# Performance work log

Measured on AMD Instinct MI355X. Metric: run time of the kernel, lower is better.

The kernel has to match this reference:

```python
import jax, jax.numpy as jnp
import numpy as np

B, S, M, D, H, L, FF = 2, 1024, 1024, 512, 8, 4, 2048
HD = D // H  # head dim 64
EPS = 1e-6   # fast_transformers linear-attention eps
LN_EPS = 1e-5


def setup_inputs() -> dict:
    key = jax.random.key(0)
    keys = iter(jax.random.split(key, 64))
    def w(shape, s=0.02):
        return jax.random.normal(next(keys), shape, dtype=jnp.float32) * s
    inp = {
        "memory": jax.random.normal(next(keys), (B, M, D), dtype=jnp.float32),
        "target": jax.random.normal(next(keys), (B, S, D), dtype=jnp.float32),
    }
    for p in ("sa", "ca"):
        for n in ("q", "k", "v", "o"):
            inp[f"{p}_W{n}"] = w((L, D, D))
            inp[f"{p}_b{n}"] = jnp.zeros((L, D), jnp.float32)
    inp["ff_W1"] = w((L, D, FF)); inp["ff_b1"] = jnp.zeros((L, FF), jnp.float32)
    inp["ff_W2"] = w((L, FF, D)); inp["ff_b2"] = jnp.zeros((L, D), jnp.float32)
    for n in ("ln1", "ln2", "ln3"):
        inp[f"{n}_g"] = jnp.ones((L, D), jnp.float32)
        inp[f"{n}_b"] = jnp.zeros((L, D), jnp.float32)
    inp["lnf_g"] = jnp.ones((D,), jnp.float32)
    inp["lnf_b"] = jnp.zeros((D,), jnp.float32)
    return inp


def _ln(x, g, b):
    m = x.mean(-1, keepdims=True)
    v = ((x - m) ** 2).mean(-1, keepdims=True)
    return (x - m) / jnp.sqrt(v + LN_EPS) * g + b


def _phi(x):  # elu feature map: elu(x) + 1
    return jax.nn.elu(x) + 1.0


def _heads(x, W, b):  # [b,s,D] -> [b,s,H,HD]
    y = x @ W + b
    return y.reshape(y.shape[0], y.shape[1], H, HD)


def _causal_linear_attn(q, k, v):
    # q,k already feature-mapped. cumulative KV state per step.
    kv = jnp.cumsum(jnp.einsum('bshd,bshm->bshdm', k, v), axis=1)  # [B,S,H,HD,HD]
    z = jnp.cumsum(k, axis=1)                                      # [B,S,H,HD]
    num = jnp.einsum('bshd,bshdm->bshm', q, kv)
    den = jnp.einsum('bshd,bshd->bsh', q, z) + EPS
    return num / den[..., None]


def _cross_linear_attn(q, k, v):
    kv = jnp.einsum('bmhd,bmhv->bhdv', k, v)  # [B,H,HD,HD]
    z = k.sum(axis=1)                          # [B,H,HD]
    num = jnp.einsum('bshd,bhdv->bshv', q, kv)
    den = jnp.einsum('bshd,bhd->bsh', q, z) + EPS
    return num / den[..., None]


def reference(memory, target,
              sa_Wq, sa_bq, sa_Wk, sa_bk, sa_Wv, sa_bv, sa_Wo, sa_bo,
              ca_Wq, ca_bq, ca_Wk, ca_bk, ca_Wv, ca_bv, ca_Wo, ca_bo,
              ff_W1, ff_b1, ff_W2, ff_b2,
              ln1_g, ln1_b, ln2_g, ln2_b, ln3_g, ln3_b, lnf_g, lnf_b):
    x = target
    for i in range(L):
        # causal linear self-attention
        q = _phi(_heads(x, sa_Wq[i], sa_bq[i]))
        k = _phi(_heads(x, sa_Wk[i], sa_bk[i]))
        v = _heads(x, sa_Wv[i], sa_bv[i])
        a = _causal_linear_attn(q, k, v).reshape(B, S, D) @ sa_Wo[i] + sa_bo[i]
        x = _ln(x + a, ln1_g[i], ln1_b[i])
        # linear cross-attention over memory
        q = _phi(_heads(x, ca_Wq[i], ca_bq[i]))
        k = _phi(_heads(memory, ca_Wk[i], ca_bk[i]))
        v = _heads(memory, ca_Wv[i], ca_bv[i])
        a = _cross_linear_attn(q, k, v).reshape(B, S, D) @ ca_Wo[i] + ca_bo[i]
        x = _ln(x + a, ln2_g[i], ln2_b[i])
        # gelu FFN
        y = jax.nn.gelu(x @ ff_W1[i] + ff_b1[i], approximate=False) @ ff_W2[i] + ff_b2[i]
        x = _ln(x + y, ln3_g[i], ln3_b[i])
    return _ln(x, lnf_g, lnf_b)
```

## Files before the change

### kernel.cpp

```cpp
#include <hip/hip_runtime.h>
#include <hip/hip_bf16.h>
#include <math.h>


typedef unsigned short u16;
typedef __bf16 bf16x8 __attribute__((ext_vector_type(8)));
typedef float f32x4v __attribute__((ext_vector_type(4)));

#define DEVI __device__ __forceinline__

DEVI float bf2f(u16 u) { return __uint_as_float(((unsigned)u) << 16); }
DEVI u16 f2bf(float f) {
  unsigned u = __float_as_uint(f);
  u += 0x7FFFu + ((u >> 16) & 1u);
  return (u16)(u >> 16);
}

__global__ __launch_bounds__(256) void transpose_f2b(
    const float* __restrict__ in, u16* __restrict__ out, int K, int N)
{
  __shared__ float tile[64 * 65];
  const size_t mat = (size_t)blockIdx.z * K * N;
  const int n0 = blockIdx.x * 64, k0 = blockIdx.y * 64;
  const int t = threadIdx.x;
#pragma unroll
  for (int p = 0; p < 16; ++p) {
    const int e = t + p * 256;
    const int lk = e >> 6, ln = e & 63;
    tile[lk * 65 + ln] = in[mat + (size_t)(k0 + lk) * N + n0 + ln];
  }
  __syncthreads();
#pragma unroll
  for (int p = 0; p < 16; ++p) {
    const int e = t + p * 256;
    const int ln = e >> 6, lk = e & 63;
    out[mat + (size_t)(n0 + ln) * K + k0 + lk] = f2bf(tile[lk * 65 + ln]);
  }
}

__global__ __launch_bounds__(256) void cast_dual(
    const float* __restrict__ in, float* __restrict__ fout, u16* __restrict__ bout)
{
  const int i = blockIdx.x * 256 + threadIdx.x;
  const float4 a = ((const float4*)in)[i * 2];
  const float4 b = ((const float4*)in)[i * 2 + 1];
  if (fout) {
    ((float4*)fout)[i * 2] = a;
    ((float4*)fout)[i * 2 + 1] = b;
  }
  ((ushort4*)bout)[i * 2]     = make_ushort4(f2bf(a.x), f2bf(a.y), f2bf(a.z), f2bf(a.w));
  ((ushort4*)bout)[i * 2 + 1] = make_ushort4(f2bf(b.x), f2bf(b.y), f2bf(b.z), f2bf(b.w));
}

template<int CDT>
__global__ __launch_bounds__(256, 4) void gemm64(
    const u16* __restrict__ A0, const u16* __restrict__ A1, const u16* __restrict__ A2,
    const u16* __restrict__ W0, const u16* __restrict__ W1, const u16* __restrict__ W2,
    const float* __restrict__ b0, const float* __restrict__ b1, const float* __restrict__ b2,
    void* __restrict__ C0, void* __restrict__ C1, void* __restrict__ C2,
    int acts, int N, int K, int lognyb)
{
  constexpr int LDT = 72;
  __shared__ __align__(16) u16 As[2][64 * LDT];
  __shared__ __align__(16) u16 Bs[2][64 * LDT];
  const int tid = threadIdx.x;
  const int by = blockIdx.y;
  const int seg = by >> lognyb;
  const int ny = by & ((1 << lognyb) - 1);
  const u16* A = seg == 0 ? A0 : (seg == 1 ? A1 : A2);
  const u16* W = seg == 0 ? W0 : (seg == 1 ? W1 : W2);
  const float* bias = seg == 0 ? b0 : (seg == 1 ? b1 : b2);
  void* Cv = seg == 0 ? C0 : (seg == 1 ? C1 : C2);
  const int act = (acts >> (2 * seg)) & 3;

  const int bm0 = blockIdx.x * 64, bn0 = ny * 64;
  const int lane = tid & 63, wid = tid >> 6;
  const int wr = wid >> 1, wc = wid & 1;
  const int l15 = lane & 15, lg = lane >> 4;
  const int srow = tid >> 2, scg = (tid & 3) * 16;
  const u16* Ap = A + (size_t)(bm0 + srow) * K + scg;
  const u16* Wp = W + (size_t)(bn0 + srow) * K + scg;

  uint4 ra0 = *(const uint4*)(Ap);
  uint4 ra1 = *(const uint4*)(Ap + 8);
  uint4 rb0 = *(const uint4*)(Wp);
  uint4 rb1 = *(const uint4*)(Wp + 8);
  *(uint4*)&As[0][srow * LDT + scg]     = ra0;
  *(uint4*)&As[0][srow * LDT + scg + 8] = ra1;
  *(uint4*)&Bs[0][srow * LDT + scg]     = rb0;
  *(uint4*)&Bs[0][srow * LDT + scg + 8] = rb1;
  __syncthreads();

  f32x4v acc[2][2] = {};
  int cur = 0;
  for (int k0 = 0; k0 < K; k0 += 64) {
    const bool more = (k0 + 64 < K);
    if (more) {
      ra0 = *(const uint4*)(Ap + k0 + 64);
      ra1 = *(const uint4*)(Ap + k0 + 72);
      rb0 = *(const uint4*)(Wp + k0 + 64);
      rb1 = *(const uint4*)(Wp + k0 + 72);
    }
    bf16x8 af[2][2], bw[2][2];
#pragma unroll
    for (int kk = 0; kk < 2; ++kk) {
#pragma unroll
      for (int mm = 0; mm < 2; ++mm)
        af[kk][mm] = *(const bf16x8*)&As[cur][(wr * 32 + mm * 16 + l15) * LDT + kk * 32 + lg * 8];
#pragma unroll
      for (int nn = 0; nn < 2; ++nn)
        bw[kk][nn] = *(const bf16x8*)&Bs[cur][(wc * 32 + nn * 16 + l15) * LDT + kk * 32 + lg * 8];
    }
#pragma unroll
    for (int kk = 0; kk < 2; ++kk)
#pragma unroll
      for (int mm = 0; mm < 2; ++mm)
#pragma unroll
        for (int nn = 0; nn < 2; ++nn)
          acc[mm][nn] = __builtin_amdgcn_mfma_f32_16x16x32_bf16(af[kk][mm], bw[kk][nn], acc[mm][nn], 0, 0, 0);
    if (more) {
      *(uint4*)&As[cur ^ 1][srow * LDT + scg]     = ra0;
      *(uint4*)&As[cur ^ 1][srow * LDT + scg + 8] = ra1;
      *(uint4*)&Bs[cur ^ 1][srow * LDT + scg]     = rb0;
      *(uint4*)&Bs[cur ^ 1][srow * LDT + scg + 8] = rb1;
    }
    __syncthreads();
    cur ^= 1;
  }
#pragma unroll
  for (int nn = 0; nn < 2; ++nn) {
    const int col = bn0 + wc * 32 + nn * 16 + l15;
    const float bv = bias[col];
#pragma unroll
    for (int mm = 0; mm < 2; ++mm) {
#pragma unroll
      for (int r = 0; r < 4; ++r) {
        const int row = bm0 + wr * 32 + mm * 16 + lg * 4 + r;
        float v = acc[mm][nn][r] + bv;
        if (act == 1) v = v > 0.f ? v + 1.f : __expf(v);
        else if (act == 2) v = 0.5f * v * (1.f + erff(v * 0.70710678f));
        if (CDT == 0) ((float*)Cv)[(size_t)row * N + col] = v;
        else          ((u16*)Cv)[(size_t)row * N + col] = f2bf(v);
      }
    }
  }
}

__global__ __launch_bounds__(256) void lin_chunk_mfma(
    const u16* __restrict__ kbuf, const u16* __restrict__ vbuf,
    float* __restrict__ KVc, float* __restrict__ zc)
{
  constexpr int LDT = 72;
  __shared__ __align__(16) u16 Kt[64 * LDT];
  __shared__ __align__(16) u16 Vt[64 * LDT];
  const int c = blockIdx.x, bh = blockIdx.y;
  const int b = bh >> 3, h = bh & 7;
  const int t = threadIdx.x;
  const size_t rowbase = (size_t)(b * 1024 + c * 64);
  const int sp = t >> 4, colq = (t & 15) * 4;
#pragma unroll
  for (int pp = 0; pp < 2; ++pp) {
    const int s0 = pp * 32 + 2 * sp;
    const ushort4 ka = *(const ushort4*)&kbuf[(rowbase + s0) * 512 + h * 64 + colq];
    const ushort4 kb_ = *(const ushort4*)&kbuf[(rowbase + s0 + 1) * 512 + h * 64 + colq];
    const ushort4 va = *(const ushort4*)&vbuf[(rowbase + s0) * 512 + h * 64 + colq];
    const ushort4 vb_ = *(const ushort4*)&vbuf[(rowbase + s0 + 1) * 512 + h * 64 + colq];
    *(unsigned*)&Kt[(colq + 0) * LDT + s0] = (unsigned)ka.x | ((unsigned)kb_.x << 16);
    *(unsigned*)&Kt[(colq + 1) * LDT + s0] = (unsigned)ka.y | ((unsigned)kb_.y << 16);
    *(unsigned*)&Kt[(colq + 2) * LDT + s0] = (unsigned)ka.z | ((unsigned)kb_.z << 16);
    *(unsigned*)&Kt[(colq + 3) * LDT + s0] = (unsigned)ka.w | ((unsigned)kb_.w << 16);
    *(unsigned*)&Vt[(colq + 0) * LDT + s0] = (unsigned)va.x | ((unsigned)vb_.x << 16);
    *(unsigned*)&Vt[(colq + 1) * LDT + s0] = (unsigned)va.y | ((unsigned)vb_.y << 16);
    *(unsigned*)&Vt[(colq + 2) * LDT + s0] = (unsigned)va.z | ((unsigned)vb_.z << 16);
    *(unsigned*)&Vt[(colq + 3) * LDT + s0] = (unsigned)va.w | ((unsigned)vb_.w << 16);
  }
  __syncthreads();
  {
    const int zd = t >> 2, zg = t & 3;
    float zp = 0.f;
#pragma unroll
    for (int ss = 0; ss < 16; ++ss) zp += bf2f(Kt[zd * LDT + zg * 16 + ss]);
    zp += __shfl_xor(zp, 1, 64);
    zp += __shfl_xor(zp, 2, 64);
    if (zg == 0) zc[(size_t)(bh * 16 + c) * 64 + zd] = zp;
  }
  const int lane = t & 63, wid = t >> 6;
  const int wr = wid >> 1, wc = wid & 1;
  const int l15 = lane & 15, lg = lane >> 4;
  bf16x8 av[2][2], bk[2][2];
#pragma unroll
  for (int kk = 0; kk < 2; ++kk) {
#pragma unroll
    for (int mm = 0; mm < 2; ++mm)
      av[kk][mm] = *(const bf16x8*)&Vt[(wr * 32 + mm * 16 + l15) * LDT + kk * 32 + lg * 8];
#pragma unroll
    for (int nn = 0; nn < 2; ++nn)
      bk[kk][nn] = *(const bf16x8*)&Kt[(wc * 32 + nn * 16 + l15) * LDT + kk * 32 + lg * 8];
  }
  f32x4v acc[2][2] = {};
#pragma unroll
  for (int kk = 0; kk < 2; ++kk)
#pragma unroll
    for (int mm = 0; mm < 2; ++mm)
#pragma unroll
      for (int nn = 0; nn < 2; ++nn)
        acc[mm][nn] = __builtin_amdgcn_mfma_f32_16x16x32_bf16(av[kk][mm], bk[kk][nn], acc[mm][nn], 0, 0, 0);
  float* kvout = KVc + (size_t)(bh * 16 + c) * 4096;
#pragma unroll
  for (int mm = 0; mm < 2; ++mm)
#pragma unroll
    for (int r = 0; r < 4; ++r) {
      const int row = wr * 32 + mm * 16 + lg * 4 + r;
#pragma unroll
      for (int nn = 0; nn < 2; ++nn) {
        const int col = wc * 32 + nn * 16 + l15;
        kvout[row * 64 + col] = acc[mm][nn][r];
      }
    }
}

__global__ __launch_bounds__(256) void lin_scan_exclusive(
    float* __restrict__ KVc, float* __restrict__ zc,
    float* __restrict__ KVtot, float* __restrict__ ztot)
{
  const int grp = blockIdx.x, bh = blockIdx.y, t = threadIdx.x;
  const size_t base = (size_t)bh * 16 * 4096 + grp * 256 + t;
  float run = 0.f;
#pragma unroll
  for (int c = 0; c < 16; ++c) {
    const float tmp = KVc[base + (size_t)c * 4096];
    KVc[base + (size_t)c * 4096] = run;
    run += tmp;
  }
  KVtot[(size_t)bh * 4096 + grp * 256 + t] = run;
  if (grp == 0 && t < 64) {
    const size_t zb = (size_t)bh * 16 * 64 + t;
    float rz = 0.f;
#pragma unroll
    for (int c = 0; c < 16; ++c) {
      const float tmp = zc[zb + c * 64];
      zc[zb + c * 64] = rz;
      rz += tmp;
    }
    ztot[bh * 64 + t] = rz;
  }
}

__global__ __launch_bounds__(256) void sa_apply_mfma(
    const u16* __restrict__ qbuf, const u16* __restrict__ kbuf,
    const u16* __restrict__ vbuf, const float* __restrict__ KVc,
    const float* __restrict__ zc, u16* __restrict__ out)
{
  constexpr int LDT = 72;
  __shared__ __align__(16) u16 Qs[64 * LDT];
  __shared__ __align__(16) u16 Ks[64 * LDT];
  __shared__ __align__(16) u16 Vt[64 * LDT];
  __shared__ __align__(16) u16 Ps[64 * LDT];
  __shared__ __align__(16) u16 KVs[64 * LDT];
  __shared__ float zp[64];
  __shared__ float den1[2][64];
  __shared__ float den2[64];
  const int c = blockIdx.x, bh = blockIdx.y;
  const int b = bh >> 3, h = bh & 7;
  const int t = threadIdx.x;
  const size_t rowbase = (size_t)(b * 1024 + c * 64);
  {
    const int srow = t >> 2, scg = (t & 3) * 16;
    *(uint4*)&Qs[srow * LDT + scg]     = *(const uint4*)&qbuf[(rowbase + srow) * 512 + h * 64 + scg];
    *(uint4*)&Qs[srow * LDT + scg + 8] = *(const uint4*)&qbuf[(rowbase + srow) * 512 + h * 64 + scg + 8];
    *(uint4*)&Ks[srow * LDT + scg]     = *(const uint4*)&kbuf[(rowbase + srow) * 512 + h * 64 + scg];
    *(uint4*)&Ks[srow * LDT + scg + 8] = *(const uint4*)&kbuf[(rowbase + srow) * 512 + h * 64 + scg + 8];
    const float* kvp = KVc + (size_t)(bh * 16 + c) * 4096 + srow * 64 + scg;
#pragma unroll
    for (int i = 0; i < 4; ++i) {
      const float4 cc = *(const float4*)&kvp[i * 4];
      *(ushort4*)&KVs[srow * LDT + scg + i * 4] = make_ushort4(f2bf(cc.x), f2bf(cc.y), f2bf(cc.z), f2bf(cc.w));
    }
  }
  {
    const int sp = t >> 4, colq = (t & 15) * 4;
#pragma unroll
    for (int pp = 0; pp < 2; ++pp) {
      const int s0 = pp * 32 + 2 * sp;
      const ushort4 va = *(const ushort4*)&vbuf[(rowbase + s0) * 512 + h * 64 + colq];
      const ushort4 vb_ = *(const ushort4*)&vbuf[(rowbase + s0 + 1) * 512 + h * 64 + colq];
      *(unsigned*)&Vt[(colq + 0) * LDT + s0] = (unsigned)va.x | ((unsigned)vb_.x << 16);
      *(unsigned*)&Vt[(colq + 1) * LDT + s0] = (unsigned)va.y | ((unsigned)vb_.y << 16);
      *(unsigned*)&Vt[(colq + 2) * LDT + s0] = (unsigned)va.z | ((unsigned)vb_.z << 16);
      *(unsigned*)&Vt[(colq + 3) * LDT + s0] = (unsigned)va.w | ((unsigned)vb_.w << 16);
    }
  }
  if (t < 64) zp[t] = zc[(size_t)(bh * 16 + c) * 64 + t];
  __syncthreads();
  {
    const int di = t >> 2, dg = t & 3;
    float p2 = 0.f;
#pragma unroll
    for (int dd = 0; dd < 16; ++dd)
      p2 += bf2f(Qs[di * LDT + dg * 16 + dd]) * zp[dg * 16 + dd];
    p2 += __shfl_xor(p2, 1, 64);
    p2 += __shfl_xor(p2, 2, 64);
    if (dg == 0) den2[di] = p2;
  }
  const int lane = t & 63, wid = t >> 6;
  const int wr = wid >> 1, wc = wid & 1;
  const int l15 = lane & 15, lg = lane >> 4;
  bf16x8 af_q[2][2], bx[2][2];
#pragma unroll
  for (int kk = 0; kk < 2; ++kk) {
#pragma unroll
    for (int mm = 0; mm < 2; ++mm)
      af_q[kk][mm] = *(const bf16x8*)&Qs[(wr * 32 + mm * 16 + l15) * LDT + kk * 32 + lg * 8];
#pragma unroll
    for (int nn = 0; nn < 2; ++nn)
      bx[kk][nn] = *(const bf16x8*)&Ks[(wc * 32 + nn * 16 + l15) * LDT + kk * 32 + lg * 8];
  }
  f32x4v s_acc[2][2] = {};
#pragma unroll
  for (int kk = 0; kk < 2; ++kk)
#pragma unroll
    for (int mm = 0; mm < 2; ++mm)
#pragma unroll
      for (int nn = 0; nn < 2; ++nn)
        s_acc[mm][nn] = __builtin_amdgcn_mfma_f32_16x16x32_bf16(af_q[kk][mm], bx[kk][nn], s_acc[mm][nn], 0, 0, 0);
#pragma unroll
  for (int mm = 0; mm < 2; ++mm)
#pragma unroll
    for (int r = 0; r < 4; ++r) {
      const int row = wr * 32 + mm * 16 + lg * 4 + r;
      float dsum = 0.f;
#pragma unroll
      for (int nn = 0; nn < 2; ++nn) {
        const int col = wc * 32 + nn * 16 + l15;
        const float val = (col <= row) ? s_acc[mm][nn][r] : 0.f;
        Ps[row * LDT + col] = f2bf(val);
        dsum += val;
      }
      dsum += __shfl_xor(dsum, 1, 64);
      dsum += __shfl_xor(dsum, 2, 64);
      dsum += __shfl_xor(dsum, 4, 64);
      dsum += __shfl_xor(dsum, 8, 64);
      if (l15 == 0) den1[wc][row] = dsum;
    }
  __syncthreads();
  bf16x8 ap[2][2];
#pragma unroll
  for (int kk = 0; kk < 2; ++kk) {
#pragma unroll
    for (int mm = 0; mm < 2; ++mm)
      ap[kk][mm] = *(const bf16x8*)&Ps[(wr * 32 + mm * 16 + l15) * LDT + kk * 32 + lg * 8];
#pragma unroll
    for (int nn = 0; nn < 2; ++nn)
      bx[kk][nn] = *(const bf16x8*)&Vt[(wc * 32 + nn * 16 + l15) * LDT + kk * 32 + lg * 8];
  }
  f32x4v o_acc[2][2] = {};
#pragma unroll
  for (int kk = 0; kk < 2; ++kk)
#pragma unroll
    for (int mm = 0; mm < 2; ++mm)
#pragma unroll
      for (int nn = 0; nn < 2; ++nn)
        o_acc[mm][nn] = __builtin_amdgcn_mfma_f32_16x16x32_bf16(ap[kk][mm], bx[kk][nn], o_acc[mm][nn], 0, 0, 0);
#pragma unroll
  for (int kk = 0; kk < 2; ++kk)
#pragma unroll
    for (int nn = 0; nn < 2; ++nn)
      bx[kk][nn] = *(const bf16x8*)&KVs[(wc * 32 + nn * 16 + l15) * LDT + kk * 32 + lg * 8];
#pragma unroll
  for (int kk = 0; kk < 2; ++kk)
#pragma unroll
    for (int mm = 0; mm < 2; ++mm)
#pragma unroll
      for (int nn = 0; nn < 2; ++nn)
        o_acc[mm][nn] = __builtin_amdgcn_mfma_f32_16x16x32_bf16(af_q[kk][mm], bx[kk][nn], o_acc[mm][nn], 0, 0, 0);
#pragma unroll
  for (int mm = 0; mm < 2; ++mm)
#pragma unroll
    for (int r = 0; r < 4; ++r) {
      const int row = wr * 32 + mm * 16 + lg * 4 + r;
      const float rden = 1.f / (den1[0][row] + den1[1][row] + den2[row] + 1e-6f);
#pragma unroll
      for (int nn = 0; nn < 2; ++nn) {
        const int col = wc * 32 + nn * 16 + l15;
        out[(rowbase + row) * 512 + h * 64 + col] = f2bf(o_acc[mm][nn][r] * rden);
      }
    }
}

__global__ __launch_bounds__(256) void ca_apply_mfma(
    const u16* __restrict__ qbuf, const float* __restrict__ KVtot,
    const float* __restrict__ ztot, u16* __restrict__ out)
{
  constexpr int LDT = 72;
  __shared__ __align__(16) u16 Qs[64 * LDT];
  __shared__ __align__(16) u16 KVs[64 * LDT];
  __shared__ float zt[64];
  __shared__ float den2[64];
  const int c = blockIdx.x, bh = blockIdx.y;
  const int b = bh >> 3, h = bh & 7;
  const int t = threadIdx.x;
  const size_t rowbase = (size_t)(b * 1024 + c * 64);
  {
    const int srow = t >> 2, scg = (t & 3) * 16;
    *(uint4*)&Qs[srow * LDT + scg]     = *(const uint4*)&qbuf[(rowbase + srow) * 512 + h * 64 + scg];
    *(uint4*)&Qs[srow * LDT + scg + 8] = *(const uint4*)&qbuf[(rowbase + srow) * 512 + h * 64 + scg + 8];
    const float* kvp = KVtot + (size_t)bh * 4096 + srow * 64 + scg;
#pragma unroll
    for (int i = 0; i < 4; ++i) {
      const float4 cc = *(const float4*)&kvp[i * 4];
      *(ushort4*)&KVs[srow * LDT + scg + i * 4] = make_ushort4(f2bf(cc.x), f2bf(cc.y), f2bf(cc.z), f2bf(cc.w));
    }
  }
  if (t < 64) zt[t] = ztot[bh * 64 + t];
  __syncthreads();
  {
    const int di = t >> 2, dg = t & 3;
    float p2 = 0.f;
#pragma unroll
    for (int dd = 0; dd < 16; ++dd)
      p2 += bf2f(Qs[di * LDT + dg * 16 + dd]) * zt[dg * 16 + dd];
    p2 += __shfl_xor(p2, 1, 64);
    p2 += __shfl_xor(p2, 2, 64);
    if (dg == 0) den2[di] = p2;
  }
  const int lane = t & 63, wid = t >> 6;
  const int wr = wid >> 1, wc = wid & 1;
  const int l15 = lane & 15, lg = lane >> 4;
  bf16x8 aq[2][2], bkv[2][2];
#pragma unroll
  for (int kk = 0; kk < 2; ++kk) {
#pragma unroll
    for (int mm = 0; mm < 2; ++mm)
      aq[kk][mm] = *(const bf16x8*)&Qs[(wr * 32 + mm * 16 + l15) * LDT + kk * 32 + lg * 8];
#pragma unroll
    for (int nn = 0; nn < 2; ++nn)
      bkv[kk][nn] = *(const bf16x8*)&KVs[(wc * 32 + nn * 16 + l15) * LDT + kk * 32 + lg * 8];
  }
  f32x4v o_acc[2][2] = {};
#pragma unroll
  for (int kk = 0; kk < 2; ++kk)
#pragma unroll
    for (int mm = 0; mm < 2; ++mm)
#pragma unroll
      for (int nn = 0; nn < 2; ++nn)
        o_acc[mm][nn] = __builtin_amdgcn_mfma_f32_16x16x32_bf16(aq[kk][mm], bkv[kk][nn], o_acc[mm][nn], 0, 0, 0);
  __syncthreads();
#pragma unroll
  for (int mm = 0; mm < 2; ++mm)
#pragma unroll
    for (int r = 0; r < 4; ++r) {
      const int row = wr * 32 + mm * 16 + lg * 4 + r;
      const float rden = 1.f / (den2[row] + 1e-6f);
#pragma unroll
      for (int nn = 0; nn < 2; ++nn) {
        const int col = wc * 32 + nn * 16 + l15;
        out[(rowbase + row) * 512 + h * 64 + col] = f2bf(o_acc[mm][nn][r] * rden);
      }
    }
}

__global__ __launch_bounds__(256) void ln_residual(
    float* __restrict__ x, const float* __restrict__ a,
    const float* __restrict__ g, const float* __restrict__ bt,
    u16* __restrict__ xb)
{
  const int t = threadIdx.x, lane = t & 63, w = t >> 6;
  const int row = blockIdx.x * 4 + w;
  float* xr = x + (size_t)row * 512;
  const float* ar = a + (size_t)row * 512;
  float4 x0 = *(const float4*)&xr[lane * 8];
  float4 x1 = *(const float4*)&xr[lane * 8 + 4];
  float4 a0 = *(const float4*)&ar[lane * 8];
  float4 a1 = *(const float4*)&ar[lane * 8 + 4];
  float v[8];
  v[0] = x0.x + a0.x; v[1] = x0.y + a0.y; v[2] = x0.z + a0.z; v[3] = x0.w + a0.w;
  v[4] = x1.x + a1.x; v[5] = x1.y + a1.y; v[6] = x1.z + a1.z; v[7] = x1.w + a1.w;
  float s = 0.f, sq = 0.f;
#pragma unroll
  for (int i = 0; i < 8; ++i) { s += v[i]; sq += v[i] * v[i]; }
#pragma unroll
  for (int off = 32; off > 0; off >>= 1) {
    s += __shfl_xor(s, off, 64);
    sq += __shfl_xor(sq, off, 64);
  }
  const float mean = s * (1.f / 512.f);
  const float var = sq * (1.f / 512.f) - mean * mean;
  const float rstd = rsqrtf(var + 1e-5f);
  float o[8];
#pragma unroll
  for (int i = 0; i < 8; ++i) {
    const int col = lane * 8 + i;
    o[i] = (v[i] - mean) * rstd * g[col] + bt[col];
  }
  *(float4*)&xr[lane * 8]     = make_float4(o[0], o[1], o[2], o[3]);
  *(float4*)&xr[lane * 8 + 4] = make_float4(o[4], o[5], o[6], o[7]);
  *(ushort4*)&xb[(size_t)row * 512 + lane * 8]     = make_ushort4(f2bf(o[0]), f2bf(o[1]), f2bf(o[2]), f2bf(o[3]));
  *(ushort4*)&xb[(size_t)row * 512 + lane * 8 + 4] = make_ushort4(f2bf(o[4]), f2bf(o[5]), f2bf(o[6]), f2bf(o[7]));
}

__global__ __launch_bounds__(256) void ln_final(
    const float* __restrict__ x, const float* __restrict__ g,
    const float* __restrict__ bt, float* __restrict__ out)
{
  const int t = threadIdx.x, lane = t & 63, w = t >> 6;
  const int row = blockIdx.x * 4 + w;
  const float* xr = x + (size_t)row * 512;
  float4 x0 = *(const float4*)&xr[lane * 8];
  float4 x1 = *(const float4*)&xr[lane * 8 + 4];
  float v[8] = { x0.x, x0.y, x0.z, x0.w, x1.x, x1.y, x1.z, x1.w };
  float s = 0.f, sq = 0.f;
#pragma unroll
  for (int i = 0; i < 8; ++i) { s += v[i]; sq += v[i] * v[i]; }
#pragma unroll
  for (int off = 32; off > 0; off >>= 1) {
    s += __shfl_xor(s, off, 64);
    sq += __shfl_xor(sq, off, 64);
  }
  const float mean = s * (1.f / 512.f);
  const float var = sq * (1.f / 512.f) - mean * mean;
  const float rstd = rsqrtf(var + 1e-5f);
  float o[8];
#pragma unroll
  for (int i = 0; i < 8; ++i) {
    const int col = lane * 8 + i;
    o[i] = (v[i] - mean) * rstd * g[col] + bt[col];
  }
  *(float4*)&out[(size_t)row * 512 + lane * 8]     = make_float4(o[0], o[1], o[2], o[3]);
  *(float4*)&out[(size_t)row * 512 + lane * 8 + 4] = make_float4(o[4], o[5], o[6], o[7]);
}

extern "C" void kernel_launch(void* const* d_in, const int* in_sizes, int n_in,
                              void* d_out, int out_size, void* d_ws, size_t ws_size,
                              hipStream_t stream)
{
  (void)in_sizes; (void)n_in; (void)out_size; (void)ws_size;
  constexpr int Dm = 512, Lc = 4, FFc = 2048;

  const float* memory = (const float*)d_in[0];
  const float* target = (const float*)d_in[1];
  const float *saW[4], *sab[4], *caW[4], *cab[4];
  for (int j = 0; j < 4; ++j) {
    saW[j] = (const float*)d_in[2 + 2 * j];
    sab[j] = (const float*)d_in[3 + 2 * j];
    caW[j] = (const float*)d_in[10 + 2 * j];
    cab[j] = (const float*)d_in[11 + 2 * j];
  }
  const float* ffW1 = (const float*)d_in[18];
  const float* ffb1 = (const float*)d_in[19];
  const float* ffW2 = (const float*)d_in[20];
  const float* ffb2 = (const float*)d_in[21];
  const float* lng[4] = { (const float*)d_in[22], (const float*)d_in[24],
                          (const float*)d_in[26], (const float*)d_in[28] };
  const float* lnb[4] = { (const float*)d_in[23], (const float*)d_in[25],
                          (const float*)d_in[27], (const float*)d_in[29] };

  size_t off = 0;
  auto alloc = [&](size_t bytes) -> void* {
    void* p = (char*)d_ws + off;
    off += (bytes + 255) & ~(size_t)255;
    return p;
  };
  u16* WtS[4]; u16* WtC[4];
  for (int j = 0; j < 4; ++j) WtS[j] = (u16*)alloc((size_t)Lc * Dm * Dm * 2);
  for (int j = 0; j < 4; ++j) WtC[j] = (u16*)alloc((size_t)Lc * Dm * Dm * 2);
  u16* WtF1 = (u16*)alloc((size_t)Lc * Dm * FFc * 2);
  u16* WtF2 = (u16*)alloc((size_t)Lc * FFc * Dm * 2);
  float* x    = (float*)alloc((size_t)2048 * 512 * 4);
  u16*   xb   = (u16*)alloc((size_t)2048 * 512 * 2);
  u16*   memb = (u16*)alloc((size_t)2048 * 512 * 2);
  u16*   qh   = (u16*)alloc((size_t)2048 * 512 * 2);
  u16*   kh   = (u16*)alloc((size_t)2048 * 512 * 2);
  u16*   vh   = (u16*)alloc((size_t)2048 * 512 * 2);
  float* resid= (float*)alloc((size_t)2048 * 512 * 4);
  u16*   attn = (u16*)alloc((size_t)2048 * 512 * 2);
  u16*   ffh  = (u16*)alloc((size_t)2048 * 2048 * 2);
  float* KVc  = (float*)alloc((size_t)16 * 16 * 4096 * 4);
  float* zcb  = (float*)alloc((size_t)16 * 16 * 64 * 4);
  float* KVtot= (float*)alloc((size_t)16 * 4096 * 4);
  float* ztot = (float*)alloc((size_t)16 * 64 * 4);

  for (int j = 0; j < 4; ++j) {
    transpose_f2b<<<dim3(8, 8, 4), 256, 0, stream>>>(saW[j], WtS[j], Dm, Dm);
    transpose_f2b<<<dim3(8, 8, 4), 256, 0, stream>>>(caW[j], WtC[j], Dm, Dm);
  }
  transpose_f2b<<<dim3(32, 8, 4), 256, 0, stream>>>(ffW1, WtF1, Dm, FFc);
  transpose_f2b<<<dim3(8, 32, 4), 256, 0, stream>>>(ffW2, WtF2, FFc, Dm);

  cast_dual<<<512, 256, 0, stream>>>(target, x, xb);
  cast_dual<<<512, 256, 0, stream>>>(memory, nullptr, memb);

  for (int i = 0; i < Lc; ++i) {
    const size_t wo  = (size_t)i * Dm * Dm;
    const size_t wo1 = (size_t)i * Dm * FFc;
    const size_t wo2 = (size_t)i * FFc * Dm;
    gemm64<1><<<dim3(32, 24), 256, 0, stream>>>(
        xb, xb, xb, WtS[0] + wo, WtS[1] + wo, WtS[2] + wo,
        sab[0] + i * Dm, sab[1] + i * Dm, sab[2] + i * Dm,
        qh, kh, vh, 0x05, 512, 512, 3);
    lin_chunk_mfma<<<dim3(16, 16), 256, 0, stream>>>(kh, vh, KVc, zcb);
    lin_scan_exclusive<<<dim3(16, 16), 256, 0, stream>>>(KVc, zcb, KVtot, ztot);
    sa_apply_mfma<<<dim3(16, 16), 256, 0, stream>>>(qh, kh, vh, KVc, zcb, attn);
    gemm64<0><<<dim3(32, 8), 256, 0, stream>>>(
        attn, attn, attn, WtS[3] + wo, WtS[3] + wo, WtS[3] + wo,
        sab[3] + i * Dm, sab[3] + i * Dm, sab[3] + i * Dm,
        resid, resid, resid, 0, 512, 512, 3);
    ln_residual<<<512, 256, 0, stream>>>(x, resid, lng[0] + i * Dm, lnb[0] + i * Dm, xb);
    gemm64<1><<<dim3(32, 24), 256, 0, stream>>>(
        xb, memb, memb, WtC[0] + wo, WtC[1] + wo, WtC[2] + wo,
        cab[0] + i * Dm, cab[1] + i * Dm, cab[2] + i * Dm,
        qh, kh, vh, 0x05, 512, 512, 3);
    lin_chunk_mfma<<<dim3(16, 16), 256, 0, stream>>>(kh, vh, KVc, zcb);
    lin_scan_exclusive<<<dim3(16, 16), 256, 0, stream>>>(KVc, zcb, KVtot, ztot);
    ca_apply_mfma<<<dim3(16, 16), 256, 0, stream>>>(qh, KVtot, ztot, attn);
    gemm64<0><<<dim3(32, 8), 256, 0, stream>>>(
        attn, attn, attn, WtC[3] + wo, WtC[3] + wo, WtC[3] + wo,
        cab[3] + i * Dm, cab[3] + i * Dm, cab[3] + i * Dm,
        resid, resid, resid, 0, 512, 512, 3);
    ln_residual<<<512, 256, 0, stream>>>(x, resid, lng[1] + i * Dm, lnb[1] + i * Dm, xb);
    gemm64<1><<<dim3(32, 32), 256, 0, stream>>>(
        xb, xb, xb, WtF1 + wo1, WtF1 + wo1, WtF1 + wo1,
        ffb1 + i * FFc, ffb1 + i * FFc, ffb1 + i * FFc,
        ffh, ffh, ffh, 2, 2048, 512, 5);
    gemm64<0><<<dim3(32, 8), 256, 0, stream>>>(
        ffh, ffh, ffh, WtF2 + wo2, WtF2 + wo2, WtF2 + wo2,
        ffb2 + i * Dm, ffb2 + i * Dm, ffb2 + i * Dm,
        resid, resid, resid, 0, 512, 2048, 3);
    ln_residual<<<512, 256, 0, stream>>>(x, resid, lng[2] + i * Dm, lnb[2] + i * Dm, xb);
  }
  ln_final<<<512, 256, 0, stream>>>(x, lng[3], lnb[3], (float*)d_out);
}
```

Measured before the change: 605.6 us.

## Use direct-to-LDS GEMM loads, larger tiles, fold scan into apply kernels

Replaces the register-staged 64x64 GEMM with a templated kernel that loads global memory straight into LDS via global_load_lds with K-step 32. The QKV and FFN1 projections move to 128x128 tiles. Separately, the exclusive-scan kernel is removed: the sa and ca apply kernels now sum the preceding chunk KV states themselves. Weight transposes for the attention matrices are batched into one launch. Launch count drops, but apply blocks do redundant prefix reads, larger tiles cut grid sizes, and the unpadded 32-wide LDS rows may bank-conflict.

```diff
diff --git a/kernel.cpp b/kernel.cpp
--- a/kernel.cpp
+++ b/kernel.cpp
@@ -14,6 +14,39 @@
   unsigned u = __float_as_uint(f);
   u += 0x7FFFu + ((u >> 16) & 1u);
   return (u16)(u >> 16);
+}
+
+DEVI void gload16(const void* g, void* lds) {
+  __builtin_amdgcn_global_load_lds(
+      (const __attribute__((address_space(1))) void*)g,
+      (__attribute__((address_space(3))) void*)lds, 16, 0, 0);
+}
+
+struct P8i { const float* p[8]; };
+struct P8o { u16* p[8]; };
+
+__global__ __launch_bounds__(256) void transpose_b8(P8i in, P8o out)
+{
+  __shared__ float tile[64 * 65];
+  const int m = blockIdx.z;
+  const int set = m >> 2, layer = m & 3;
+  const float* src = in.p[set] + (size_t)layer * 512 * 512;
+  u16* dst = out.p[set] + (size_t)layer * 512 * 512;
+  const int n0 = blockIdx.x * 64, k0 = blockIdx.y * 64;
+  const int t = threadIdx.x;
+#pragma unroll
+  for (int p = 0; p < 16; ++p) {
+    const int e = t + p * 256;
+    const int lk = e >> 6, ln = e & 63;
+    tile[lk * 65 + ln] = src[(size_t)(k0 + lk) * 512 + n0 + ln];
+  }
+  __syncthreads();
+#pragma unroll
+  for (int p = 0; p < 16; ++p) {
+    const int e = t + p * 256;
+    const int ln = e >> 6, lk = e & 63;
+    dst[(size_t)(n0 + ln) * 512 + k0 + lk] = f2bf(tile[lk * 65 + ln]);
+  }
 }
 
 __global__ __launch_bounds__(256) void transpose_f2b(
@@ -52,17 +85,17 @@
   ((ushort4*)bout)[i * 2 + 1] = make_ushort4(f2bf(b.x), f2bf(b.y), f2bf(b.z), f2bf(b.w));
 }
 
-template<int CDT>
-__global__ __launch_bounds__(256, 4) void gemm64(
+template<int BM, int BN, int CDT>
+__global__ __launch_bounds__(256) void gemmT(
     const u16* __restrict__ A0, const u16* __restrict__ A1, const u16* __restrict__ A2,
     const u16* __restrict__ W0, const u16* __restrict__ W1, const u16* __restrict__ W2,
     const float* __restrict__ b0, const float* __restrict__ b1, const float* __restrict__ b2,
     void* __restrict__ C0, void* __restrict__ C1, void* __restrict__ C2,
     int acts, int N, int K, int lognyb)
 {
-  constexpr int LDT = 72;
-  __shared__ __align__(16) u16 As[2][64 * LDT];
-  __shared__ __align__(16) u16 Bs[2][64 * LDT];
+  constexpr int NM = BM / 32, NN = BN / 32;
+  __shared__ __align__(16) u16 As[2][BM * 32];
+  __shared__ __align__(16) u16 Bs[2][BN * 32];
   const int tid = threadIdx.x;
   const int by = blockIdx.y;
   const int seg = by >> lognyb;
@@ -73,69 +106,55 @@
   void* Cv = seg == 0 ? C0 : (seg == 1 ? C1 : C2);
   const int act = (acts >> (2 * seg)) & 3;
 
-  const int bm0 = blockIdx.x * 64, bn0 = ny * 64;
+  const int bm0 = blockIdx.x * BM, bn0 = ny * BN;
   const int lane = tid & 63, wid = tid >> 6;
   const int wr = wid >> 1, wc = wid & 1;
   const int l15 = lane & 15, lg = lane >> 4;
-  const int srow = tid >> 2, scg = (tid & 3) * 16;
-  const u16* Ap = A + (size_t)(bm0 + srow) * K + scg;
-  const u16* Wp = W + (size_t)(bn0 + srow) * K + scg;
-
-  uint4 ra0 = *(const uint4*)(Ap);
-  uint4 ra1 = *(const uint4*)(Ap + 8);
-  uint4 rb0 = *(const uint4*)(Wp);
-  uint4 rb1 = *(const uint4*)(Wp + 8);
-  *(uint4*)&As[0][srow * LDT + scg]     = ra0;
-  *(uint4*)&As[0][srow * LDT + scg + 8] = ra1;
-  *(uint4*)&Bs[0][srow * LDT + scg]     = rb0;
-  *(uint4*)&Bs[0][srow * LDT + scg + 8] = rb1;
-  __syncthreads();
-
-  f32x4v acc[2][2] = {};
+  const int rl = lane >> 2, col8 = (lane & 3) * 8;
+
+  auto stage = [&](int buf, int k0) {
+#pragma unroll
+    for (int p = 0; p < BM / 64; ++p) {
+      const int ch = wid + 4 * p;
+      gload16(&A[(size_t)(bm0 + ch * 16 + rl) * K + k0 + col8], &As[buf][ch * 512]);
+    }
+#pragma unroll
+    for (int p = 0; p < BN / 64; ++p) {
+      const int ch = wid + 4 * p;
+      gload16(&W[(size_t)(bn0 + ch * 16 + rl) * K + k0 + col8], &Bs[buf][ch * 512]);
+    }
+  };
+
+  stage(0, 0);
+  __syncthreads();
+  f32x4v acc[NM][NN] = {};
   int cur = 0;
-  for (int k0 = 0; k0 < K; k0 += 64) {
-    const bool more = (k0 + 64 < K);
-    if (more) {
-      ra0 = *(const uint4*)(Ap + k0 + 64);
-      ra1 = *(const uint4*)(Ap + k0 + 72);
-      rb0 = *(const uint4*)(Wp + k0 + 64);
-      rb1 = *(const uint4*)(Wp + k0 + 72);
-    }
-    bf16x8 af[2][2], bw[2][2];
-#pragma unroll
-    for (int kk = 0; kk < 2; ++kk) {
-#pragma unroll
-      for (int mm = 0; mm < 2; ++mm)
-        af[kk][mm] = *(const bf16x8*)&As[cur][(wr * 32 + mm * 16 + l15) * LDT + kk * 32 + lg * 8];
-#pragma unroll
-      for (int nn = 0; nn < 2; ++nn)
-        bw[kk][nn] = *(const bf16x8*)&Bs[cur][(wc * 32 + nn * 16 + l15) * LDT + kk * 32 + lg * 8];
-    }
-#pragma unroll
-    for (int kk = 0; kk < 2; ++kk)
-#pragma unroll
-      for (int mm = 0; mm < 2; ++mm)
-#pragma unroll
-        for (int nn = 0; nn < 2; ++nn)
-          acc[mm][nn] = __builtin_amdgcn_mfma_f32_16x16x32_bf16(af[kk][mm], bw[kk][nn], acc[mm][nn], 0, 0, 0);
-    if (more) {
-      *(uint4*)&As[cur ^ 1][srow * LDT + scg]     = ra0;
-      *(uint4*)&As[cur ^ 1][srow * LDT + scg + 8] = ra1;
-      *(uint4*)&Bs[cur ^ 1][srow * LDT + scg]     = rb0;
-      *(uint4*)&Bs[cur ^ 1][srow * LDT + scg + 8] = rb1;
-    }
+  for (int k0 = 0; k0 < K; k0 += 32) {
+    if (k0 + 32 < K) stage(cur ^ 1, k0 + 32);
+    bf16x8 af[NM], bw[NN];
+#pragma unroll
+    for (int mm = 0; mm < NM; ++mm)
+      af[mm] = *(const bf16x8*)&As[cur][(wr * (BM / 2) + mm * 16 + l15) * 32 + lg * 8];
+#pragma unroll
+    for (int nn = 0; nn < NN; ++nn)
+      bw[nn] = *(const bf16x8*)&Bs[cur][(wc * (BN / 2) + nn * 16 + l15) * 32 + lg * 8];
+#pragma unroll
+    for (int mm = 0; mm < NM; ++mm)
+#pragma unroll
+      for (int nn = 0; nn < NN; ++nn)
+        acc[mm][nn] = __builtin_amdgcn_mfma_f32_16x16x32_bf16(af[mm], bw[nn], acc[mm][nn], 0, 0, 0);
     __syncthreads();
     cur ^= 1;
   }
 #pragma unroll
-  for (int nn = 0; nn < 2; ++nn) {
-    const int col = bn0 + wc * 32 + nn * 16 + l15;
+  for (int nn = 0; nn < NN; ++nn) {
+    const int col = bn0 + wc * (BN / 2) + nn * 16 + l15;
     const float bv = bias[col];
 #pragma unroll
-    for (int mm = 0; mm < 2; ++mm) {
+    for (int mm = 0; mm < NM; ++mm) {
 #pragma unroll
       for (int r = 0; r < 4; ++r) {
-        const int row = bm0 + wr * 32 + mm * 16 + lg * 4 + r;
+        const int row = bm0 + wr * (BM / 2) + mm * 16 + lg * 4 + r;
         float v = acc[mm][nn][r] + bv;
         if (act == 1) v = v > 0.f ? v + 1.f : __expf(v);
         else if (act == 2) v = 0.5f * v * (1.f + erff(v * 0.70710678f));
@@ -217,33 +236,6 @@
         kvout[row * 64 + col] = acc[mm][nn][r];
       }
     }
-}
-
-__global__ __launch_bounds__(256) void lin_scan_exclusive(
-    float* __restrict__ KVc, float* __restrict__ zc,
-    float* __restrict__ KVtot, float* __restrict__ ztot)
-{
-  const int grp = blockIdx.x, bh = blockIdx.y, t = threadIdx.x;
-  const size_t base = (size_t)bh * 16 * 4096 + grp * 256 + t;
-  float run = 0.f;
-#pragma unroll
-  for (int c = 0; c < 16; ++c) {
-    const float tmp = KVc[base + (size_t)c * 4096];
-    KVc[base + (size_t)c * 4096] = run;
-    run += tmp;
-  }
-  KVtot[(size_t)bh * 4096 + grp * 256 + t] = run;
-  if (grp == 0 && t < 64) {
-    const size_t zb = (size_t)bh * 16 * 64 + t;
-    float rz = 0.f;
-#pragma unroll
-    for (int c = 0; c < 16; ++c) {
-      const float tmp = zc[zb + c * 64];
-      zc[zb + c * 64] = rz;
-      rz += tmp;
-    }
-    ztot[bh * 64 + t] = rz;
-  }
 }
 
 __global__ __launch_bounds__(256) void sa_apply_mfma(
@@ -270,12 +262,23 @@
     *(uint4*)&Qs[srow * LDT + scg + 8] = *(const uint4*)&qbuf[(rowbase + srow) * 512 + h * 64 + scg + 8];
     *(uint4*)&Ks[srow * LDT + scg]     = *(const uint4*)&kbuf[(rowbase + srow) * 512 + h * 64 + scg];
     *(uint4*)&Ks[srow * LDT + scg + 8] = *(const uint4*)&kbuf[(rowbase + srow) * 512 + h * 64 + scg + 8];
-    const float* kvp = KVc + (size_t)(bh * 16 + c) * 4096 + srow * 64 + scg;
-#pragma unroll
-    for (int i = 0; i < 4; ++i) {
-      const float4 cc = *(const float4*)&kvp[i * 4];
-      *(ushort4*)&KVs[srow * LDT + scg + i * 4] = make_ushort4(f2bf(cc.x), f2bf(cc.y), f2bf(cc.z), f2bf(cc.w));
-    }
+    const float* kvbase = KVc + (size_t)(bh * 16) * 4096 + srow * 64 + scg;
+    float4 s0 = make_float4(0, 0, 0, 0), s1 = s0, s2 = s0, s3 = s0;
+    for (int cc = 0; cc < c; ++cc) {
+      const float* p = kvbase + (size_t)cc * 4096;
+      const float4 a0 = *(const float4*)&p[0];
+      const float4 a1 = *(const float4*)&p[4];
+      const float4 a2 = *(const float4*)&p[8];
+      const float4 a3 = *(const float4*)&p[12];
+      s0.x += a0.x; s0.y += a0.y; s0.z += a0.z; s0.w += a0.w;
+      s1.x += a1.x; s1.y += a1.y; s1.z += a1.z; s1.w += a1.w;
+      s2.x += a2.x; s2.y += a2.y; s2.z += a2.z; s2.w += a2.w;
+      s3.x += a3.x; s3.y += a3.y; s3.z += a3.z; s3.w += a3.w;
+    }
+    *(ushort4*)&KVs[srow * LDT + scg + 0]  = make_ushort4(f2bf(s0.x), f2bf(s0.y), f2bf(s0.z), f2bf(s0.w));
+    *(ushort4*)&KVs[srow * LDT + scg + 4]  = make_ushort4(f2bf(s1.x), f2bf(s1.y), f2bf(s1.z), f2bf(s1.w));
+    *(ushort4*)&KVs[srow * LDT + scg + 8]  = make_ushort4(f2bf(s2.x), f2bf(s2.y), f2bf(s2.z), f2bf(s2.w));
+    *(ushort4*)&KVs[srow * LDT + scg + 12] = make_ushort4(f2bf(s3.x), f2bf(s3.y), f2bf(s3.z), f2bf(s3.w));
   }
   {
     const int sp = t >> 4, colq = (t & 15) * 4;
@@ -290,7 +293,11 @@
       *(unsigned*)&Vt[(colq + 3) * LDT + s0] = (unsigned)va.w | ((unsigned)vb_.w << 16);
     }
   }
-  if (t < 64) zp[t] = zc[(size_t)(bh * 16 + c) * 64 + t];
+  if (t < 64) {
+    float z = 0.f;
+    for (int cc = 0; cc < c; ++cc) z += zc[(size_t)(bh * 16 + cc) * 64 + t];
+    zp[t] = z;
+  }
   __syncthreads();
   {
     const int di = t >> 2, dg = t & 3;
@@ -388,8 +395,8 @@
 }
 
 __global__ __launch_bounds__(256) void ca_apply_mfma(
-    const u16* __restrict__ qbuf, const float* __restrict__ KVtot,
-    const float* __restrict__ ztot, u16* __restrict__ out)
+    const u16* __restrict__ qbuf, const float* __restrict__ KVc,
+    const float* __restrict__ zc, u16* __restrict__ out)
 {
   constexpr int LDT = 72;
   __shared__ __align__(16) u16 Qs[64 * LDT];
@@ -404,14 +411,29 @@
     const int srow = t >> 2, scg = (t & 3) * 16;
     *(uint4*)&Qs[srow * LDT + scg]     = *(const uint4*)&qbuf[(rowbase + srow) * 512 + h * 64 + scg];
     *(uint4*)&Qs[srow * LDT + scg + 8] = *(const uint4*)&qbuf[(rowbase + srow) * 512 + h * 64 + scg + 8];
-    const float* kvp = KVtot + (size_t)bh * 4096 + srow * 64 + scg;
-#pragma unroll
-    for (int i = 0; i < 4; ++i) {
-      const float4 cc = *(const float4*)&kvp[i * 4];
-      *(ushort4*)&KVs[srow * LDT + scg + i * 4] = make_ushort4(f2bf(cc.x), f2bf(cc.y), f2bf(cc.z), f2bf(cc.w));
-    }
-  }
-  if (t < 64) zt[t] = ztot[bh * 64 + t];
+    const float* kvbase = KVc + (size_t)(bh * 16) * 4096 + srow * 64 + scg;
+    float4 s0 = make_float4(0, 0, 0, 0), s1 = s0, s2 = s0, s3 = s0;
+    for (int cc = 0; cc < 16; ++cc) {
+      const float* p = kvbase + (size_t)cc * 4096;
+      const float4 a0 = *(const float4*)&p[0];
+      const float4 a1 = *(const float4*)&p[4];
+      const float4 a2 = *(const float4*)&p[8];
+      const float4 a3 = *(const float4*)&p[12];
+      s0.x += a0.x; s0.y += a0.y; s0.z += a0.z; s0.w += a0.w;
+      s1.x += a1.x; s1.y += a1.y; s1.z += a1.z; s1.w += a1.w;
+      s2.x += a2.x; s2.y += a2.y; s2.z += a2.z; s2.w += a2.w;
+      s3.x += a3.x; s3.y += a3.y; s3.z += a3.z; s3.w += a3.w;
+    }
+    *(ushort4*)&KVs[srow * LDT + scg + 0]  = make_ushort4(f2bf(s0.x), f2bf(s0.y), f2bf(s0.z), f2bf(s0.w));
+    *(ushort4*)&KVs[srow * LDT + scg + 4]  = make_ushort4(f2bf(s1.x), f2bf(s1.y), f2bf(s1.z), f2bf(s1.w));
+    *(ushort4*)&KVs[srow * LDT + scg + 8]  = make_ushort4(f2bf(s2.x), f2bf(s2.y), f2bf(s2.z), f2bf(s2.w));
+    *(ushort4*)&KVs[srow * LDT + scg + 12] = make_ushort4(f2bf(s3.x), f2bf(s3.y), f2bf(s3.z), f2bf(s3.w));
+  }
+  if (t < 64) {
+    float z = 0.f;
+    for (int cc = 0; cc < 16; ++cc) z += zc[(size_t)(bh * 16 + cc) * 64 + t];
+    zt[t] = z;
+  }
   __syncthreads();
   {
     const int di = t >> 2, dg = t & 3;
@@ -576,12 +598,12 @@
   u16*   ffh  = (u16*)alloc((size_t)2048 * 2048 * 2);
   float* KVc  = (float*)alloc((size_t)16 * 16 * 4096 * 4);
   float* zcb  = (float*)alloc((size_t)16 * 16 * 64 * 4);
-  float* KVtot= (float*)alloc((size_t)16 * 4096 * 4);
-  float* ztot = (float*)alloc((size_t)16 * 64 * 4);
-
-  for (int j = 0; j < 4; ++j) {
-    transpose_f2b<<<dim3(8, 8, 4), 256, 0, stream>>>(saW[j], WtS[j], Dm, Dm);
-    transpose_f2b<<<dim3(8, 8, 4), 256, 0, stream>>>(caW[j], WtC[j], Dm, Dm);
+
+  {
+    P8i pin; P8o pout;
+    for (int j = 0; j < 4; ++j) { pin.p[j] = saW[j]; pout.p[j] = WtS[j]; }
+    for (int j = 0; j < 4; ++j) { pin.p[4 + j] = caW[j]; pout.p[4 + j] = WtC[j]; }
+    transpose_b8<<<dim3(8, 8, 32), 256, 0, stream>>>(pin, pout);
   }
   transpose_f2b<<<dim3(32, 8, 4), 256, 0, stream>>>(ffW1, WtF1, Dm, FFc);
   transpose_f2b<<<dim3(8, 32, 4), 256, 0, stream>>>(ffW2, WtF2, FFc, Dm);
@@ -593,35 +615,33 @@
     const size_t wo  = (size_t)i * Dm * Dm;
     const size_t wo1 = (size_t)i * Dm * FFc;
     const size_t wo2 = (size_t)i * FFc * Dm;
-    gemm64<1><<<dim3(32, 24), 256, 0, stream>>>(
+    gemmT<128, 128, 1><<<dim3(16, 12), 256, 0, stream>>>(
         xb, xb, xb, WtS[0] + wo, WtS[1] + wo, WtS[2] + wo,
         sab[0] + i * Dm, sab[1] + i * Dm, sab[2] + i * Dm,
-        qh, kh, vh, 0x05, 512, 512, 3);
+        qh, kh, vh, 0x05, 512, 512, 2);
     lin_chunk_mfma<<<dim3(16, 16), 256, 0, stream>>>(kh, vh, KVc, zcb);
-    lin_scan_exclusive<<<dim3(16, 16), 256, 0, stream>>>(KVc, zcb, KVtot, ztot);
     sa_apply_mfma<<<dim3(16, 16), 256, 0, stream>>>(qh, kh, vh, KVc, zcb, attn);
-    gemm64<0><<<dim3(32, 8), 256, 0, stream>>>(
+    gemmT<64, 64, 0><<<dim3(32, 8), 256, 0, stream>>>(
         attn, attn, attn, WtS[3] + wo, WtS[3] + wo, WtS[3] + wo,
         sab[3] + i * Dm, sab[3] + i * Dm, sab[3] + i * Dm,
         resid, resid, resid, 0, 512, 512, 3);
     ln_residual<<<512, 256, 0, stream>>>(x, resid, lng[0] + i * Dm, lnb[0] + i * Dm, xb);
-    gemm64<1><<<dim3(32, 24), 256, 0, stream>>>(
+    gemmT<128, 128, 1><<<dim3(16, 12), 256, 0, stream>>>(
         xb, memb, memb, WtC[0] + wo, WtC[1] + wo, WtC[2] + wo,
         cab[0] + i * Dm, cab[1] + i * Dm, cab[2] + i * Dm,
-        qh, kh, vh, 0x05, 512, 512, 3);
+        qh, kh, vh, 0x05, 512, 512, 2);
     lin_chunk_mfma<<<dim3(16, 16), 256, 0, stream>>>(kh, vh, KVc, zcb);
-    lin_scan_exclusive<<<dim3(16, 16), 256, 0, stream>>>(KVc, zcb, KVtot, ztot);
-    ca_apply_mfma<<<dim3(16, 16), 256, 0, stream>>>(qh, KVtot, ztot, attn);
-    gemm64<0><<<dim3(32, 8), 256, 0, stream>>>(
+    ca_apply_mfma<<<dim3(16, 16), 256, 0, stream>>>(qh, KVc, zcb, attn);
+    gemmT<64, 64, 0><<<dim3(32, 8), 256, 0, stream>>>(
         attn, attn, attn, WtC[3] + wo, WtC[3] + wo, WtC[3] + wo,
         cab[3] + i * Dm, cab[3] + i * Dm, cab[3] + i * Dm,
         resid, resid, resid, 0, 512, 512, 3);
     ln_residual<<<512, 256, 0, stream>>>(x, resid, lng[1] + i * Dm, lnb[1] + i * Dm, xb);
-    gemm64<1><<<dim3(32, 32), 256, 0, stream>>>(
+    gemmT<128, 128, 1><<<dim3(16, 16), 256, 0, stream>>>(
         xb, xb, xb, WtF1 + wo1, WtF1 + wo1, WtF1 + wo1,
         ffb1 + i * FFc, ffb1 + i * FFc, ffb1 + i * FFc,
-        ffh, ffh, ffh, 2, 2048, 512, 5);
-    gemm64<0><<<dim3(32, 8), 256, 0, stream>>>(
+        ffh, ffh, ffh, 2, 2048, 512, 4);
+    gemmT<64, 64, 0><<<dim3(32, 8), 256, 0, stream>>>(
         ffh, ffh, ffh, WtF2 + wo2, WtF2 + wo2, WtF2 + wo2,
         ffb2 + i * Dm, ffb2 + i * Dm, ffb2 + i * Dm,
         resid, resid, resid, 0, 512, 2048, 3);
```

Result: slower. 745.8 us (+23.2%).
